# Performance work log

Measured on AMD Instinct MI355X. Metric: run time of the kernel, lower is better.

## Reference

```python
import jax, jax.numpy as jnp
import numpy as np

B, L, D = 256, 64, 1024


def setup_inputs() -> dict:
    key = jax.random.key(0)
    k0, k1, k2, k3, k4, k5, k6 = jax.random.split(key, 7)
    left = jax.random.normal(k0, (B, L, D), jnp.float32)
    right = jax.random.normal(k1, (B, L, D), jnp.float32)
    s = 1.0 / np.sqrt(L)  # torch Linear default init bound
    Wl = jax.random.uniform(k2, (L, L), jnp.float32, -s, s)
    bl = jax.random.uniform(k3, (L,), jnp.float32, -s, s)
    Wr = jax.random.uniform(k4, (L, L), jnp.float32, -s, s)
    br = jax.random.uniform(k5, (L,), jnp.float32, -s, s)
    sc = 1.0 / np.sqrt(2 * L * 3)  # Conv1d(2L->L, k=3) default init bound
    Wconv = jax.random.uniform(k6, (L, 2 * L, 3), jnp.float32, -sc, sc)
    return {"left": left, "right": right, "Wl": Wl, "bl": bl,
            "Wr": Wr, "br": br, "Wconv": Wconv}


def reference(left, right, Wl, bl, Wr, br, Wconv):
    Bd, Ld, Dd = left.shape
    # nn.Linear(L,L) over the length axis: y[b,k,d] = sum_l x[b,l,d] * W[k,l] + b[k]
    left = jnp.einsum('bld,kl->bkd', left, Wl) + bl[None, :, None]
    right = jnp.einsum('bld,kl->bkd', right, Wr) + br[None, :, None]
    # The 2L-step python loop computes, for i in [0, 2L):
    #   out[:, i, :] = sum_j left[:, j, :] * right[:, j + (L-1) - i, :]  (in-range j)
    # i.e. a full cross-correlation along the length axis (last row all zeros).
    # lax conv IS cross-correlation, so run one grouped conv over B*D channels.
    lhs = left.transpose(0, 2, 1).reshape(1, Bd * Dd, Ld)    # [1, B*D, L]  (NCW)
    rhs = right.transpose(0, 2, 1).reshape(Bd * Dd, 1, Ld)   # [B*D, 1, L]  (OIW)
    corr = jax.lax.conv_general_dilated(
        lhs, rhs, window_strides=(1,), padding=[(Ld - 1, Ld - 1)],
        dimension_numbers=('NCW', 'OIW', 'NCW'),
        feature_group_count=Bd * Dd)                          # [1, B*D, 2L-1]
    corr = jnp.pad(corr, ((0, 0), (0, 0), (0, 1)))            # last shift is all-zero
    out = corr.reshape(Bd, Dd, 2 * Ld).transpose(0, 2, 1)     # [B, 2L, D]
    # nn.Conv1d(2L -> L, kernel_size=3, padding=1, bias=False), width = D
    y = jax.lax.conv_general_dilated(
        out, Wconv, window_strides=(1,), padding=[(1, 1)],
        dimension_numbers=('NCW', 'OIW', 'NCW'))              # [B, L, D]
    return y
```

## Files before the change

kernel.cpp:

```cpp
#include <hip/hip_runtime.h>

#define DD 1024
#define TD 62
#define NTILE 17
#define BB 256

typedef __attribute__((ext_vector_type(8))) short short8;
typedef __attribute__((ext_vector_type(4))) float float4_;

__device__ __forceinline__ unsigned short f2bf(float f) {
    union { float f; unsigned u; } v; v.f = f;
    unsigned u = v.u;
    return (unsigned short)((u + 0x7fffu + ((u >> 16) & 1u)) >> 16);
}
__device__ __forceinline__ unsigned pack2(float a, float b) {
    return (unsigned)f2bf(a) | ((unsigned)f2bf(b) << 16);
}

__global__ void prep_w(const float* __restrict__ Wconv,
                       const float* __restrict__ Wl,
                       const float* __restrict__ Wr,
                       unsigned short* __restrict__ W2) {
    int o = blockIdx.x * 256 + threadIdx.x;
    if (o < 24576) {
        int j = o & 7, lane = (o >> 3) & 63, w = (o >> 9) & 3, q = (o >> 11) & 3, t = o >> 13;
        int m = lane & 15, quad = lane >> 4;
        int k = 16 * w + m, c = 32 * q + 8 * quad + j;
        W2[o] = f2bf(Wconv[(k * 128 + c) * 3 + t]);
    } else {
        int o2 = o - 24576;
        int j = o2 & 7, lane = (o2 >> 3) & 63, mt = (o2 >> 9) & 3,
            l0s = (o2 >> 11) & 1, mat = (o2 >> 12) & 1;
        int m = lane & 15, quad = lane >> 4;
        int k = 16 * mt + m, l = 32 * l0s + quad * 8 + j;
        const float* src = mat ? Wr : Wl;
        W2[o] = f2bf(src[k * 64 + l]);
    }
}

template<int W>
__device__ __forceinline__ void corrAB(const float (&L)[64][64], const float (&Rr)[64],
                                       float (&accA)[16], float (&accB)[16], int lane) {
#pragma unroll
    for (int ii = 0; ii < 16; ++ii) { accA[ii] = 0.0f; accB[ii] = 0.0f; }
#pragma unroll
    for (int j = 0; j < 64; ++j) {
        float Lj = L[j][lane];
#pragma unroll
        for (int ii = 0; ii < 16; ++ii) {
            const int i = 16 * W + ii;
            if (j <= i) accA[ii] += Lj * Rr[j + 63 - i];
            else        accB[ii] += Lj * Rr[j - 1 - i];
        }
    }
}

template<bool PRE>
__global__ __launch_bounds__(256, 3)
void fused_cc_kernel(const float* __restrict__ left,
                     const float* __restrict__ right,
                     const float* __restrict__ Wl,
                     const float* __restrict__ bl,
                     const float* __restrict__ Wr,
                     const float* __restrict__ br,
                     const float* __restrict__ Wconv,
                     const unsigned short* __restrict__ W2,
                     float* __restrict__ out) {
    __shared__ float bufL[64][64];
    __shared__ float bufR[64][64];
    __shared__ unsigned sh[4224];

    unsigned* xL = sh;
    unsigned* xR = sh + 2048;
    unsigned short* corrT = (unsigned short*)sh;

    const int tid  = threadIdx.x;
    const int lane = tid & 63;
    const int w    = __builtin_amdgcn_readfirstlane(tid >> 6);
    const int kw   = 16 * w;
    const int m16  = lane & 15;
    const int quad = lane >> 4;

    const int b       = blockIdx.y;
    const int d_start = blockIdx.x * TD;
    const int ncols   = min(TD, DD - d_start);

    const int  g        = d_start - 1 + lane;
    const bool colvalid = (g >= 0) && (g < DD);

    if (tid < 128) sh[4096 + tid] = 0u;

    const float* lb = left  + (size_t)b * 64 * DD;
    const float* rb = right + (size_t)b * 64 * DD;

#pragma unroll
    for (int i = 0; i < 8; ++i) {
        int p = 8 * w + i, l = 2 * p;
        float a0 = colvalid ? lb[l * DD + g] : 0.0f;
        float a1 = colvalid ? lb[(l + 1) * DD + g] : 0.0f;
        float c0 = colvalid ? rb[l * DD + g] : 0.0f;
        float c1 = colvalid ? rb[(l + 1) * DD + g] : 0.0f;
        xL[p * 64 + lane] = pack2(a0, a1);
        xR[p * 64 + lane] = pack2(c0, c1);
    }
    __syncthreads();

    short8 afL[2], afR[2];
    if (PRE) {
        const short8* Wf = (const short8*)(W2 + 24576);
        afL[0] = Wf[(0 * 4 + w) * 64 + lane];
        afL[1] = Wf[(1 * 4 + w) * 64 + lane];
        afR[0] = Wf[(2 * 4 + w) * 64 + lane];
        afR[1] = Wf[(3 * 4 + w) * 64 + lane];
    } else {
#pragma unroll
        for (int l0s = 0; l0s < 2; ++l0s) {
            const float* pL = Wl + (kw + m16) * 64 + 32 * l0s + quad * 8;
            const float* pR = Wr + (kw + m16) * 64 + 32 * l0s + quad * 8;
#pragma unroll
            for (int j = 0; j < 8; ++j) {
                afL[l0s][j] = (short)f2bf(pL[j]);
                afR[l0s][j] = (short)f2bf(pR[j]);
            }
        }
    }
    float4_ accL[4], accR[4];
#pragma unroll
    for (int nt = 0; nt < 4; ++nt) { accL[nt] = (float4_){0,0,0,0}; accR[nt] = (float4_){0,0,0,0}; }
#pragma unroll
    for (int l0s = 0; l0s < 2; ++l0s)
#pragma unroll
        for (int nt = 0; nt < 4; ++nt) {
            union { unsigned u[4]; short8 s; } tL, tR;
#pragma unroll
            for (int jj = 0; jj < 4; ++jj) {
                int a = (l0s * 16 + quad * 4 + jj) * 64 + nt * 16 + m16;
                tL.u[jj] = xL[a];
                tR.u[jj] = xR[a];
            }
            accL[nt] = __builtin_amdgcn_mfma_f32_16x16x32_bf16(afL[l0s], tL.s, accL[nt], 0, 0, 0);
            accR[nt] = __builtin_amdgcn_mfma_f32_16x16x32_bf16(afR[l0s], tR.s, accR[nt], 0, 0, 0);
        }

    float blv[4], brv[4];
#pragma unroll
    for (int r = 0; r < 4; ++r) {
        int krow = kw + quad * 4 + r;
        blv[r] = bl[krow]; brv[r] = br[krow];
    }
#pragma unroll
    for (int nt = 0; nt < 4; ++nt)
#pragma unroll
        for (int r = 0; r < 4; ++r) {
            int krow = kw + quad * 4 + r, col = nt * 16 + m16;
            bufL[krow][col] = accL[nt][r] + blv[r];
            bufR[krow][col] = accR[nt][r] + brv[r];
        }
    __syncthreads();

    float Rr[64];
#pragma unroll
    for (int j = 0; j < 64; ++j) Rr[j] = bufR[j][lane];

    float accA[16], accB[16];
    switch (w) {
        case 0: corrAB<0>(bufL, Rr, accA, accB, lane); break;
        case 1: corrAB<1>(bufL, Rr, accA, accB, lane); break;
        case 2: corrAB<2>(bufL, Rr, accA, accB, lane); break;
        default: corrAB<3>(bufL, Rr, accA, accB, lane); break;
    }
    {
        const float* srcs[4] = { accA, accA + 8, accB, accB + 8 };
        const int grps[4] = { 2 * w, 2 * w + 1, 8 + 2 * w, 8 + 2 * w + 1 };
#pragma unroll
        for (int s = 0; s < 4; ++s) {
            short8 v;
#pragma unroll
            for (int j = 0; j < 8; ++j) v[j] = colvalid ? (short)f2bf(srcs[s][j]) : (short)0;
            int phys = grps[s] ^ (lane & 7);
            *(short8*)&corrT[lane * 128 + phys * 8] = v;
        }
    }
    __syncthreads();

    short8 af[12];
#pragma unroll
    for (int t = 0; t < 3; ++t)
#pragma unroll
        for (int qi = 0; qi < 4; ++qi) {
            if (PRE) {
                af[t * 4 + qi] = ((const short8*)W2)[((t * 4 + qi) * 4 + w) * 64 + lane];
            } else {
                const float* p = Wconv + ((kw + m16) * 128 + 32 * qi + 8 * quad) * 3 + t;
#pragma unroll
                for (int j = 0; j < 8; ++j) af[t * 4 + qi][j] = (short)f2bf(p[3 * j]);
            }
        }
    float4_ yacc[4];
#pragma unroll
    for (int nt = 0; nt < 4; ++nt) yacc[nt] = (float4_){0,0,0,0};
#pragma unroll
    for (int t = 0; t < 3; ++t)
#pragma unroll
        for (int qi = 0; qi < 4; ++qi)
#pragma unroll
            for (int nt = 0; nt < 4; ++nt) {
                int row  = nt * 16 + m16 + t;
                int phys = (4 * qi + quad) ^ (row & 7);
                short8 bf = *(const short8*)&corrT[row * 128 + phys * 8];
                yacc[nt] = __builtin_amdgcn_mfma_f32_16x16x32_bf16(af[t * 4 + qi], bf,
                                                                   yacc[nt], 0, 0, 0);
            }

#pragma unroll
    for (int nt = 0; nt < 4; ++nt) {
        const int dd = nt * 16 + m16;
        if (dd < ncols) {
#pragma unroll
            for (int r = 0; r < 4; ++r) {
                int k = kw + 4 * quad + r;
                out[((size_t)b * 64 + k) * DD + d_start + dd] = yacc[nt][r];
            }
        }
    }
}

extern "C" void kernel_launch(void* const* d_in, const int* in_sizes, int n_in,
                              void* d_out, int out_size, void* d_ws, size_t ws_size,
                              hipStream_t stream) {
    const float* left  = (const float*)d_in[0];
    const float* right = (const float*)d_in[1];
    const float* Wl    = (const float*)d_in[2];
    const float* bl    = (const float*)d_in[3];
    const float* Wr    = (const float*)d_in[4];
    const float* br    = (const float*)d_in[5];
    const float* Wconv = (const float*)d_in[6];
    float* out = (float*)d_out;

    dim3 grid(NTILE, BB);
    if (ws_size >= 32768 * sizeof(unsigned short)) {
        unsigned short* W2 = (unsigned short*)d_ws;
        prep_w<<<128, 256, 0, stream>>>(Wconv, Wl, Wr, W2);
        fused_cc_kernel<true><<<grid, dim3(256), 0, stream>>>(left, right, Wl, bl, Wr, br,
                                                              Wconv, W2, out);
    } else {
        fused_cc_kernel<false><<<grid, dim3(256), 0, stream>>>(left, right, Wl, bl, Wr, br,
                                                               Wconv, nullptr, out);
    }
}
```

Before: 242.3 us.

## Store projected L/R in packed fp16 shared buffers and raise occupancy target

Shrinks shared memory by storing the linear-projected left/right activations as packed fp16 pairs with XOR swizzles instead of fp32 64x64 tiles. The shared footprint drops to 32KB, so launch bounds can move from 3 to 4 blocks per CU. The global load of inputs now comes after the weight-fragment load, and the corrT write is moved after the conv weight loads. It risks reduced precision, since values go through fp16, and register pressure under the tighter occupancy bound. There is also a possible race: corrT aliases xL/xR while other waves may still be reading Lh.

```diff
diff --git a/kernel.cpp b/kernel.cpp
--- a/kernel.cpp
+++ b/kernel.cpp
@@ -15,6 +15,17 @@
 }
 __device__ __forceinline__ unsigned pack2(float a, float b) {
     return (unsigned)f2bf(a) | ((unsigned)f2bf(b) << 16);
+}
+__device__ __forceinline__ unsigned packh2(float a, float b) {
+    union { _Float16 h[2]; unsigned u; } v;
+    v.h[0] = (_Float16)a; v.h[1] = (_Float16)b;
+    return v.u;
+}
+__device__ __forceinline__ float h2f_lo(unsigned u) {
+    union { unsigned u; _Float16 h[2]; } v; v.u = u; return (float)v.h[0];
+}
+__device__ __forceinline__ float h2f_hi(unsigned u) {
+    union { unsigned u; _Float16 h[2]; } v; v.u = u; return (float)v.h[1];
 }
 
 __global__ void prep_w(const float* __restrict__ Wconv,
@@ -39,24 +50,30 @@
 }
 
 template<int W>
-__device__ __forceinline__ void corrAB(const float (&L)[64][64], const float (&Rr)[64],
+__device__ __forceinline__ void corrAB(const unsigned* __restrict__ Lh, const float (&Rr)[64],
                                        float (&accA)[16], float (&accB)[16], int lane) {
 #pragma unroll
     for (int ii = 0; ii < 16; ++ii) { accA[ii] = 0.0f; accB[ii] = 0.0f; }
 #pragma unroll
-    for (int j = 0; j < 64; ++j) {
-        float Lj = L[j][lane];
-#pragma unroll
-        for (int ii = 0; ii < 16; ++ii) {
-            const int i = 16 * W + ii;
-            if (j <= i) accA[ii] += Lj * Rr[j + 63 - i];
-            else        accB[ii] += Lj * Rr[j - 1 - i];
+    for (int j2 = 0; j2 < 32; ++j2) {
+        unsigned u = Lh[j2 * 64 + (lane ^ (((j2 >> 1) & 1) << 4))];
+        float Lj0 = h2f_lo(u), Lj1 = h2f_hi(u);
+#pragma unroll
+        for (int jj = 0; jj < 2; ++jj) {
+            const int j = 2 * j2 + jj;
+            const float Lj = jj ? Lj1 : Lj0;
+#pragma unroll
+            for (int ii = 0; ii < 16; ++ii) {
+                const int i = 16 * W + ii;
+                if (j <= i) accA[ii] += Lj * Rr[j + 63 - i];
+                else        accB[ii] += Lj * Rr[j - 1 - i];
+            }
         }
     }
 }
 
 template<bool PRE>
-__global__ __launch_bounds__(256, 3)
+__global__ __launch_bounds__(256, 4)
 void fused_cc_kernel(const float* __restrict__ left,
                      const float* __restrict__ right,
                      const float* __restrict__ Wl,
@@ -66,13 +83,12 @@
                      const float* __restrict__ Wconv,
                      const unsigned short* __restrict__ W2,
                      float* __restrict__ out) {
-    __shared__ float bufL[64][64];
-    __shared__ float bufR[64][64];
-    __shared__ unsigned sh[4224];
-
-    unsigned* xL = sh;
-    unsigned* xR = sh + 2048;
-    unsigned short* corrT = (unsigned short*)sh;
+    __shared__ unsigned shm[8192];
+    unsigned* xL = shm;
+    unsigned* xR = shm + 2048;
+    unsigned* Lh = shm + 4096;
+    unsigned* Rh = shm + 6144;
+    unsigned short* corrT = (unsigned short*)shm;
 
     const int tid  = threadIdx.x;
     const int lane = tid & 63;
@@ -88,22 +104,8 @@
     const int  g        = d_start - 1 + lane;
     const bool colvalid = (g >= 0) && (g < DD);
 
-    if (tid < 128) sh[4096 + tid] = 0u;
-
     const float* lb = left  + (size_t)b * 64 * DD;
     const float* rb = right + (size_t)b * 64 * DD;
-
-#pragma unroll
-    for (int i = 0; i < 8; ++i) {
-        int p = 8 * w + i, l = 2 * p;
-        float a0 = colvalid ? lb[l * DD + g] : 0.0f;
-        float a1 = colvalid ? lb[(l + 1) * DD + g] : 0.0f;
-        float c0 = colvalid ? rb[l * DD + g] : 0.0f;
-        float c1 = colvalid ? rb[(l + 1) * DD + g] : 0.0f;
-        xL[p * 64 + lane] = pack2(a0, a1);
-        xR[p * 64 + lane] = pack2(c0, c1);
-    }
-    __syncthreads();
 
     short8 afL[2], afR[2];
     if (PRE) {
@@ -124,64 +126,73 @@
             }
         }
     }
-    float4_ accL[4], accR[4];
-#pragma unroll
-    for (int nt = 0; nt < 4; ++nt) { accL[nt] = (float4_){0,0,0,0}; accR[nt] = (float4_){0,0,0,0}; }
-#pragma unroll
-    for (int l0s = 0; l0s < 2; ++l0s)
-#pragma unroll
-        for (int nt = 0; nt < 4; ++nt) {
-            union { unsigned u[4]; short8 s; } tL, tR;
-#pragma unroll
-            for (int jj = 0; jj < 4; ++jj) {
-                int a = (l0s * 16 + quad * 4 + jj) * 64 + nt * 16 + m16;
-                tL.u[jj] = xL[a];
-                tR.u[jj] = xR[a];
-            }
-            accL[nt] = __builtin_amdgcn_mfma_f32_16x16x32_bf16(afL[l0s], tL.s, accL[nt], 0, 0, 0);
-            accR[nt] = __builtin_amdgcn_mfma_f32_16x16x32_bf16(afR[l0s], tR.s, accR[nt], 0, 0, 0);
-        }
-
     float blv[4], brv[4];
 #pragma unroll
     for (int r = 0; r < 4; ++r) {
         int krow = kw + quad * 4 + r;
         blv[r] = bl[krow]; brv[r] = br[krow];
     }
-#pragma unroll
-    for (int nt = 0; nt < 4; ++nt)
-#pragma unroll
-        for (int r = 0; r < 4; ++r) {
-            int krow = kw + quad * 4 + r, col = nt * 16 + m16;
-            bufL[krow][col] = accL[nt][r] + blv[r];
-            bufR[krow][col] = accR[nt][r] + brv[r];
-        }
+
+#pragma unroll
+    for (int i = 0; i < 8; ++i) {
+        int p = 8 * w + i, l = 2 * p;
+        float a0 = colvalid ? lb[l * DD + g] : 0.0f;
+        float a1 = colvalid ? lb[(l + 1) * DD + g] : 0.0f;
+        float c0 = colvalid ? rb[l * DD + g] : 0.0f;
+        float c1 = colvalid ? rb[(l + 1) * DD + g] : 0.0f;
+        int pc = lane ^ (((p >> 2) & 1) << 4);
+        xL[p * 64 + pc] = pack2(a0, a1);
+        xR[p * 64 + pc] = pack2(c0, c1);
+    }
     __syncthreads();
 
+    float4_ accL[4], accR[4];
+#pragma unroll
+    for (int nt = 0; nt < 4; ++nt) { accL[nt] = (float4_){0,0,0,0}; accR[nt] = (float4_){0,0,0,0}; }
+#pragma unroll
+    for (int l0s = 0; l0s < 2; ++l0s)
+#pragma unroll
+        for (int nt = 0; nt < 4; ++nt) {
+            union { unsigned u[4]; short8 s; } tL, tR;
+#pragma unroll
+            for (int jj = 0; jj < 4; ++jj) {
+                int row = l0s * 16 + quad * 4 + jj;
+                int col = (nt * 16 + m16) ^ (((row >> 2) & 1) << 4);
+                int a = row * 64 + col;
+                tL.u[jj] = xL[a];
+                tR.u[jj] = xR[a];
+            }
+            accL[nt] = __builtin_amdgcn_mfma_f32_16x16x32_bf16(afL[l0s], tL.s, accL[nt], 0, 0, 0);
+            accR[nt] = __builtin_amdgcn_mfma_f32_16x16x32_bf16(afR[l0s], tR.s, accR[nt], 0, 0, 0);
+        }
+
+#pragma unroll
+    for (int nt = 0; nt < 4; ++nt) {
+        int col = nt * 16 + m16;
+        int k2  = 8 * w + 2 * quad;
+        int c0 = col ^ ((quad & 1) << 4);
+        Lh[k2 * 64 + c0]       = packh2(accL[nt][0] + blv[0], accL[nt][1] + blv[1]);
+        Lh[(k2 + 1) * 64 + c0] = packh2(accL[nt][2] + blv[2], accL[nt][3] + blv[3]);
+        Rh[k2 * 64 + c0]       = packh2(accR[nt][0] + brv[0], accR[nt][1] + brv[1]);
+        Rh[(k2 + 1) * 64 + c0] = packh2(accR[nt][2] + brv[2], accR[nt][3] + brv[3]);
+    }
+    __syncthreads();
+
     float Rr[64];
 #pragma unroll
-    for (int j = 0; j < 64; ++j) Rr[j] = bufR[j][lane];
+    for (int k2 = 0; k2 < 32; ++k2) {
+        unsigned u = Rh[k2 * 64 + (lane ^ (((k2 >> 1) & 1) << 4))];
+        Rr[2 * k2]     = h2f_lo(u);
+        Rr[2 * k2 + 1] = h2f_hi(u);
+    }
 
     float accA[16], accB[16];
     switch (w) {
-        case 0: corrAB<0>(bufL, Rr, accA, accB, lane); break;
-        case 1: corrAB<1>(bufL, Rr, accA, accB, lane); break;
-        case 2: corrAB<2>(bufL, Rr, accA, accB, lane); break;
-        default: corrAB<3>(bufL, Rr, accA, accB, lane); break;
-    }
-    {
-        const float* srcs[4] = { accA, accA + 8, accB, accB + 8 };
-        const int grps[4] = { 2 * w, 2 * w + 1, 8 + 2 * w, 8 + 2 * w + 1 };
-#pragma unroll
-        for (int s = 0; s < 4; ++s) {
-            short8 v;
-#pragma unroll
-            for (int j = 0; j < 8; ++j) v[j] = colvalid ? (short)f2bf(srcs[s][j]) : (short)0;
-            int phys = grps[s] ^ (lane & 7);
-            *(short8*)&corrT[lane * 128 + phys * 8] = v;
-        }
-    }
-    __syncthreads();
+        case 0: corrAB<0>(Lh, Rr, accA, accB, lane); break;
+        case 1: corrAB<1>(Lh, Rr, accA, accB, lane); break;
+        case 2: corrAB<2>(Lh, Rr, accA, accB, lane); break;
+        default: corrAB<3>(Lh, Rr, accA, accB, lane); break;
+    }
 
     short8 af[12];
 #pragma unroll
@@ -196,6 +207,21 @@
                 for (int j = 0; j < 8; ++j) af[t * 4 + qi][j] = (short)f2bf(p[3 * j]);
             }
         }
+
+    {
+        const float* srcs[4] = { accA, accA + 8, accB, accB + 8 };
+        const int grps[4] = { 2 * w, 2 * w + 1, 8 + 2 * w, 8 + 2 * w + 1 };
+#pragma unroll
+        for (int s = 0; s < 4; ++s) {
+            short8 v;
+#pragma unroll
+            for (int j = 0; j < 8; ++j) v[j] = colvalid ? (short)f2bf(srcs[s][j]) : (short)0;
+            int phys = grps[s] ^ (lane & 7);
+            *(short8*)&corrT[lane * 128 + phys * 8] = v;
+        }
+    }
+    __syncthreads();
+
     float4_ yacc[4];
 #pragma unroll
     for (int nt = 0; nt < 4; ++nt) yacc[nt] = (float4_){0,0,0,0};
```

Result: slower. 315.1 us (+30.0%).
